# Kernel optimization log

Hardware: AMD Instinct MI355X
Metric: run time of the kernel (lower is better)

The kernel has to match this reference:

```python
import jax, jax.numpy as jnp
import numpy as np

N_CLASS, EMB, NH = 32000, 256, 512
B, T = 128, 256


def setup_inputs() -> dict:
    key = jax.random.key(0)
    ks = jax.random.split(key, 16)
    s_e = 1.0 / np.sqrt(EMB)
    s_h = 1.0 / np.sqrt(NH)
    inp = {
        "X": jax.random.randint(ks[0], (B, T), 0, N_CLASS),
        "H": jax.random.normal(ks[1], (B, NH), jnp.float32),
        "C": jax.random.normal(ks[2], (B, NH), jnp.float32),
        "E": jax.random.normal(ks[3], (N_CLASS, EMB), jnp.float32),
        # Linear weights stored as (in, out) so forward is x @ W
        "Wxf": jax.random.normal(ks[4], (EMB, NH), jnp.float32) * s_e,
        "Whf": jax.random.normal(ks[5], (NH, NH), jnp.float32) * s_h,
        "bf": jnp.ones((NH,), jnp.float32),
        "Wxi": jax.random.normal(ks[6], (EMB, NH), jnp.float32) * s_e,
        "Whi": jax.random.normal(ks[7], (NH, NH), jnp.float32) * s_h,
        "bi": jnp.ones((NH,), jnp.float32),
        "Wxc": jax.random.normal(ks[8], (EMB, NH), jnp.float32) * s_e,
        "Whc": jax.random.normal(ks[9], (NH, NH), jnp.float32) * s_h,
        "bc": jnp.ones((NH,), jnp.float32),
        "Wxo": jax.random.normal(ks[10], (EMB, NH), jnp.float32) * s_e,
        "Who": jax.random.normal(ks[11], (NH, NH), jnp.float32) * s_h,
        "bo": jnp.ones((NH,), jnp.float32),
        "Whq": jax.random.normal(ks[12], (NH, N_CLASS), jnp.float32) * s_h,
        "bq": jnp.ones((N_CLASS,), jnp.float32),
    }
    return inp


def reference(X, H, C, E, Wxf, Whf, bf, Wxi, Whi, bi, Wxc, Whc, bc,
              Wxo, Who, bo, Whq, bq):
    Xe = E[X]                      # [B, T, EMB]
    Xe = jnp.swapaxes(Xe, 0, 1)    # [T, B, EMB]
    # Precompute all input-side gate projections in one big GEMM pass.
    Wx = jnp.concatenate([Wxf, Wxi, Wxc, Wxo], axis=1)   # [EMB, 4*NH]
    gx = jnp.einsum('tbe,eg->tbg', Xe, Wx)               # [T, B, 4*NH]

    def step(carry, gxt):
        H, C = carry
        gf, gi, gc, go = jnp.split(gxt, 4, axis=-1)
        Ft = jax.nn.sigmoid(gf + H @ Whf + bf)
        It = jax.nn.sigmoid(gi + H @ Whi + bi)
        Ct = jnp.tanh(gc + H @ Whc + bc)
        Ot = jax.nn.sigmoid(go + H @ Who + bo)
        # NOTE: original code updates H with the OLD C, then updates C.
        Hn = Ot * jnp.tanh(C)
        Cn = Ft * C + It * Ct
        return (Hn, Cn), None

    (H, C), _ = jax.lax.scan(step, (H, C), gx)
    return H @ Whq + bq            # [B, N_CLASS]
```

## Files before the change

kernel.cpp:

```cpp
#include <hip/hip_runtime.h>
#include <stdint.h>

#define NCLASS 32000
#define EMB    256
#define NH     512
#define BATCH  128
#define TSEQ   256
#define G4     2048
#define NGROUP 8
#define NSLICE 32
#define GROWS  16

typedef _Float16 f16;
typedef _Float16 half8  __attribute__((ext_vector_type(8)));
typedef _Float16 half4v __attribute__((ext_vector_type(4)));
typedef float    float4v __attribute__((ext_vector_type(4)));

__device__ __forceinline__ float sigm(float x) { return 1.f / (1.f + __expf(-x)); }
__device__ __forceinline__ float ftanh(float x) {
    float a = fabsf(x);
    float e = __expf(2.f * a);
    float r = 1.f - 2.f / (e + 1.f);
    return copysignf(r, x);
}

#define GLOAD64_SC0(dst, ap) asm volatile("global_load_dwordx2 %0, %1, off sc0" : "=v"(dst) : "v"(ap))
#define GLOAD32_SC0(dst, ap) asm volatile("global_load_dword %0, %1, off sc0" : "=v"(dst) : "v"(ap))
#define GSTORE32_SC0(ap, val) asm volatile("global_store_dword %0, %1, off sc0" :: "v"(ap), "v"(val) : "memory")
#define WAITVM0() asm volatile("s_waitcnt vmcnt(0)" ::: "memory")


__global__ __launch_bounds__(256) void pack_wT(
    const float* __restrict__ Wf, const float* __restrict__ Wi,
    const float* __restrict__ Wc, const float* __restrict__ Wo,
    f16* __restrict__ WT, int K)
{
    int idx = blockIdx.x * 256 + threadIdx.x;
    if (idx >= G4 * K) return;
    int c = idx / K, k = idx - c * K;
    int j = c >> 2, g = c & 3;
    const float* W = (g == 0) ? Wf : ((g == 1) ? Wi : ((g == 2) ? Wc : Wo));
    WT[idx] = (f16)W[k * NH + j];
}

__global__ __launch_bounds__(256) void pack_bias(
    const float* __restrict__ bf_, const float* __restrict__ bi_,
    const float* __restrict__ bc_, const float* __restrict__ bo_,
    float* __restrict__ br)
{
    int c = blockIdx.x * 256 + threadIdx.x;
    if (c >= G4) return;
    int j = c >> 2, g = c & 3;
    const float* b = (g == 0) ? bf_ : ((g == 1) ? bi_ : ((g == 2) ? bc_ : bo_));
    br[c] = b[j];
}

__global__ __launch_bounds__(256) void transp_whq(
    const float* __restrict__ Whq, f16* __restrict__ WqT)
{
    __shared__ f16 T[64][72];
    int tid = threadIdx.x;
    int nb = blockIdx.x % (NCLASS / 64);
    int kb = blockIdx.x / (NCLASS / 64);
    int n0 = nb * 64, k0 = kb * 64;
    #pragma unroll
    for (int r = 0; r < 16; r++) {
        int id = tid + r * 256;
        int kr = id >> 6, nc = id & 63;
        T[nc][kr] = (f16)Whq[(size_t)(k0 + kr) * NCLASS + n0 + nc];
    }
    __syncthreads();
    #pragma unroll
    for (int r = 0; r < 2; r++) {
        int id = tid + r * 256;
        int nr = id >> 3, kc = (id & 7) * 8;
        *(half8*)&WqT[(size_t)(n0 + nr) * NH + k0 + kc] = *(half8*)&T[nr][kc];
    }
}

__global__ __launch_bounds__(256) void init_h(
    const float* __restrict__ H, f16* __restrict__ Hh)
{
    int i = blockIdx.x * 256 + threadIdx.x;
    if (i >= BATCH * NH) return;
    Hh[i] = (f16)H[i];
}

__global__ void zero_sync(int* s) { s[threadIdx.x] = 0; s[threadIdx.x + 256] = 0; }

__global__ __launch_bounds__(256) void lstm_persist(
    const int* __restrict__ X, const float* __restrict__ E,
    const float* __restrict__ C0,
    const f16* __restrict__ WxT, const f16* __restrict__ WhT,
    const float* __restrict__ bias,
    f16* __restrict__ Hb0, f16* __restrict__ Hb1,
    int* __restrict__ sync)
{
    __shared__ f16 WhS[64][520];
    __shared__ f16 WxS[64][264];
    __shared__ f16 XeS[2][16][264];
    __shared__ f16 HS[16][520];
    __shared__ int sGrp[2];

    const int tid  = threadIdx.x;
    const int wave = tid >> 6, lane = tid & 63;
    const int lrow = lane & 15, lhi = lane >> 4;
    const int gg = lane & 3;
    const int uu = (lane >> 2) & 3;

    if (tid == 0) {
        uint32_t xcc;
        asm volatile("s_getreg_b32 %0, hwreg(HW_REG_XCC_ID)" : "=s"(xcc));
        int grp = (int)(xcc & 7);
        sGrp[0] = grp;
        sGrp[1] = atomicAdd(&sync[256 + grp * 32], 1);
    }
    __syncthreads();
    const int g  = sGrp[0];
    const int s  = sGrp[1] & 31;
    const int b0 = g * GROWS;
    const int c0 = s * 64;
    const int j0 = s * 16;
    int* fl = sync + g * NSLICE;

    #pragma unroll
    for (int r = 0; r < 16; r++) {
        int id = tid + r * 256;
        int row = id >> 6, ko = (id & 63) * 8;
        *(half8*)&WhS[row][ko] = *(const half8*)(WhT + (size_t)(c0 + row) * NH + ko);
    }
    #pragma unroll
    for (int r = 0; r < 8; r++) {
        int id = tid + r * 256;
        int row = id >> 5, ko = (id & 31) * 8;
        *(half8*)&WxS[row][ko] = *(const half8*)(WxT + (size_t)(c0 + row) * EMB + ko);
    }
    float cReg = C0[(size_t)(b0 + 4 * lhi + gg) * NH + j0 + wave * 4 + uu];
    const float bv = bias[c0 + wave * 16 + lrow];

    auto prefetch_xe = [&](int t, int slot) {
        #pragma unroll
        for (int r = 0; r < 4; r++) {
            int id = tid + r * 256;
            int row = id >> 6, k4 = id & 63;
            int xv = X[(size_t)(b0 + row) * TSEQ + t];
            float4v e = *(const float4v*)(E + (size_t)xv * EMB + k4 * 4);
            half4v h; h[0] = (f16)e[0]; h[1] = (f16)e[1]; h[2] = (f16)e[2]; h[3] = (f16)e[3];
            *(half4v*)&XeS[slot][row][k4 * 4] = h;
        }
    };

    float4v acc0, acc1, acc2, acc3;
    auto mfma_wx = [&](int slot) {
        acc0 = (float4v)0.f; acc1 = (float4v)0.f;
        acc2 = (float4v)0.f; acc3 = (float4v)0.f;
        const f16(*xp)[264] = XeS[slot];
        #pragma unroll
        for (int kk = 0; kk < EMB; kk += 128) {
            half8 a0 = *(const half8*)&xp[lrow][kk      + lhi * 8];
            half8 w0 = *(const half8*)&WxS[wave * 16 + lrow][kk      + lhi * 8];
            half8 a1 = *(const half8*)&xp[lrow][kk + 32 + lhi * 8];
            half8 w1 = *(const half8*)&WxS[wave * 16 + lrow][kk + 32 + lhi * 8];
            half8 a2 = *(const half8*)&xp[lrow][kk + 64 + lhi * 8];
            half8 w2 = *(const half8*)&WxS[wave * 16 + lrow][kk + 64 + lhi * 8];
            half8 a3 = *(const half8*)&xp[lrow][kk + 96 + lhi * 8];
            half8 w3 = *(const half8*)&WxS[wave * 16 + lrow][kk + 96 + lhi * 8];
            acc0 = __builtin_amdgcn_mfma_f32_16x16x32_f16(a0, w0, acc0, 0, 0, 0);
            acc1 = __builtin_amdgcn_mfma_f32_16x16x32_f16(a1, w1, acc1, 0, 0, 0);
            acc2 = __builtin_amdgcn_mfma_f32_16x16x32_f16(a2, w2, acc2, 0, 0, 0);
            acc3 = __builtin_amdgcn_mfma_f32_16x16x32_f16(a3, w3, acc3, 0, 0, 0);
        }
    };

    prefetch_xe(0, 0);
    __syncthreads();
    mfma_wx(0);
    prefetch_xe(1, 1);

    for (int t = 0; t < TSEQ; t++) {
        if (wave == 0) {
            uint64_t fap = (uint64_t)(fl + (lane & 31));
            int f;
            do {
                GLOAD32_SC0(f, fap);
                WAITVM0();
                if (lane >= 32) f = 0x7fffffff;
            } while (__all(f >= t) == 0);
        }
        __syncthreads();

        {
            const f16* hsrcp = (t & 1) ? Hb1 : Hb0;
            uint64_t hv0, hv1, hv2, hv3, hv4, hv5, hv6, hv7;
#define LDH(rr, vv) { const int id_ = tid + rr * 256; const int row_ = id_ >> 7, qc_ = id_ & 127; \
            uint64_t ap_ = (uint64_t)(hsrcp + (size_t)(b0 + row_) * NH + qc_ * 4); GLOAD64_SC0(vv, ap_); }
            LDH(0, hv0) LDH(1, hv1) LDH(2, hv2) LDH(3, hv3)
            LDH(4, hv4) LDH(5, hv5) LDH(6, hv6) LDH(7, hv7)
#undef LDH
            WAITVM0();
            __builtin_amdgcn_sched_barrier(0);
#define STH(rr, vv) { const int id_ = tid + rr * 256; const int row_ = id_ >> 7, qc_ = id_ & 127; \
            *(uint64_t*)((char*)&HS[row_][0] + (size_t)qc_ * 8) = vv; }
            STH(0, hv0) STH(1, hv1) STH(2, hv2) STH(3, hv3)
            STH(4, hv4) STH(5, hv5) STH(6, hv6) STH(7, hv7)
#undef STH
        }
        __syncthreads();

        #pragma unroll
        for (int kk = 0; kk < NH; kk += 128) {
            half8 a0 = *(const half8*)&HS[lrow][kk      + lhi * 8];
            half8 w0 = *(const half8*)&WhS[wave * 16 + lrow][kk      + lhi * 8];
            half8 a1 = *(const half8*)&HS[lrow][kk + 32 + lhi * 8];
            half8 w1 = *(const half8*)&WhS[wave * 16 + lrow][kk + 32 + lhi * 8];
            half8 a2 = *(const half8*)&HS[lrow][kk + 64 + lhi * 8];
            half8 w2 = *(const half8*)&WhS[wave * 16 + lrow][kk + 64 + lhi * 8];
            half8 a3 = *(const half8*)&HS[lrow][kk + 96 + lhi * 8];
            half8 w3 = *(const half8*)&WhS[wave * 16 + lrow][kk + 96 + lhi * 8];
            acc0 = __builtin_amdgcn_mfma_f32_16x16x32_f16(a0, w0, acc0, 0, 0, 0);
            acc1 = __builtin_amdgcn_mfma_f32_16x16x32_f16(a1, w1, acc1, 0, 0, 0);
            acc2 = __builtin_amdgcn_mfma_f32_16x16x32_f16(a2, w2, acc2, 0, 0, 0);
            acc3 = __builtin_amdgcn_mfma_f32_16x16x32_f16(a3, w3, acc3, 0, 0, 0);
        }

        {
            float4v ssum = acc0 + acc1 + acc2 + acc3;
            ssum[0] += bv; ssum[1] += bv; ssum[2] += bv; ssum[3] += bv;
            float sg  = gg == 0 ? ssum[0] : gg == 1 ? ssum[1] : gg == 2 ? ssum[2] : ssum[3];
            float sg1 = gg == 0 ? ssum[1] : gg == 1 ? ssum[0] : gg == 2 ? ssum[3] : ssum[2];
            float sg2 = gg == 0 ? ssum[2] : gg == 1 ? ssum[3] : gg == 2 ? ssum[0] : ssum[1];
            float sg3 = gg == 0 ? ssum[3] : gg == 1 ? ssum[2] : gg == 2 ? ssum[1] : ssum[0];
            float r1 = __shfl_xor(sg1, 1);
            float r2 = __shfl_xor(sg2, 2);
            float r3 = __shfl_xor(sg3, 3);
            float F  = gg == 0 ? sg : gg == 1 ? r1 : gg == 2 ? r2 : r3;
            float I  = gg == 0 ? r1 : gg == 1 ? sg : gg == 2 ? r3 : r2;
            float Cc = gg == 0 ? r2 : gg == 1 ? r3 : gg == 2 ? sg : r1;
            float O  = gg == 0 ? r3 : gg == 1 ? r2 : gg == 2 ? r1 : sg;

            float Hn = sigm(O) * ftanh(cReg);
            cReg = sigm(F) * cReg + sigm(I) * ftanh(Cc);

            float Hp = __shfl_xor(Hn, 4);
            if ((lane & 4) == 0) {
                union { f16 h[2]; uint32_t u32; } pk;
                pk.h[0] = (f16)Hn; pk.h[1] = (f16)Hp;
                f16* hb = ((t + 1) & 1) ? Hb1 : Hb0;
                const int brow = b0 + 4 * lhi + gg;
                const int jcol = j0 + wave * 4 + uu;
                uint64_t ap = (uint64_t)(hb + (size_t)brow * NH + jcol);
                GSTORE32_SC0(ap, pk.u32);
            }
        }
        WAITVM0();
        __syncthreads();

        if (tid == 0)
            GSTORE32_SC0((uint64_t)&fl[s], t + 1);

        if (t + 1 < TSEQ) {
            mfma_wx((t + 1) & 1);
            if (t + 2 < TSEQ) prefetch_xe(t + 2, t & 1);
        }
    }
}

__global__ __launch_bounds__(256) void gemm_out(
    const f16* __restrict__ Hh, const f16* __restrict__ WqT,
    const float* __restrict__ bq, float* __restrict__ out)
{
    __shared__ f16 As[128][40];
    __shared__ f16 BsT[64][40];
    int tid = threadIdx.x, wave = tid >> 6, lane = tid & 63;
    int lrow = lane & 15, lhi = lane >> 4;
    int col0 = blockIdx.x * 64;

    float4v acc[2][4];
    #pragma unroll
    for (int m = 0; m < 2; m++)
        #pragma unroll
        for (int j = 0; j < 4; j++) acc[m][j] = (float4v)0.f;

    int ar = tid >> 1, ako = (tid & 1) * 16;
    int br = tid >> 2, bko = (tid & 3) * 8;
    for (int kk = 0; kk < NH; kk += 32) {
        *(half8*)&As[ar][ako]     = *(const half8*)(Hh + (size_t)ar * NH + kk + ako);
        *(half8*)&As[ar][ako + 8] = *(const half8*)(Hh + (size_t)ar * NH + kk + ako + 8);
        *(half8*)&BsT[br][bko]    = *(const half8*)(WqT + (size_t)(col0 + br) * NH + kk + bko);
        __syncthreads();
        half8 af[2];
        #pragma unroll
        for (int m = 0; m < 2; m++)
            af[m] = *(const half8*)&As[wave * 32 + m * 16 + lrow][lhi * 8];
        #pragma unroll
        for (int j = 0; j < 4; j++) {
            half8 bfr = *(const half8*)&BsT[j * 16 + lrow][lhi * 8];
            #pragma unroll
            for (int m = 0; m < 2; m++)
                acc[m][j] = __builtin_amdgcn_mfma_f32_16x16x32_f16(af[m], bfr, acc[m][j], 0, 0, 0);
        }
        __syncthreads();
    }
    #pragma unroll
    for (int m = 0; m < 2; m++)
        #pragma unroll
        for (int j = 0; j < 4; j++) {
            int col = col0 + j * 16 + lrow;
            float bqv = bq[col];
            #pragma unroll
            for (int r = 0; r < 4; r++) {
                int row = wave * 32 + m * 16 + lhi * 4 + r;
                out[(size_t)row * NCLASS + col] = acc[m][j][r] + bqv;
            }
        }
}

extern "C" void kernel_launch(void* const* d_in, const int* in_sizes, int n_in,
                              void* d_out, int out_size, void* d_ws, size_t ws_size,
                              hipStream_t stream)
{
    (void)in_sizes; (void)n_in; (void)out_size;
    const int*   X   = (const int*)  d_in[0];
    const float* H0  = (const float*)d_in[1];
    const float* C0  = (const float*)d_in[2];
    const float* E   = (const float*)d_in[3];
    const float* Wxf = (const float*)d_in[4];
    const float* Whf = (const float*)d_in[5];
    const float* bf_ = (const float*)d_in[6];
    const float* Wxi = (const float*)d_in[7];
    const float* Whi = (const float*)d_in[8];
    const float* bi_ = (const float*)d_in[9];
    const float* Wxc = (const float*)d_in[10];
    const float* Whc = (const float*)d_in[11];
    const float* bc_ = (const float*)d_in[12];
    const float* Wxo = (const float*)d_in[13];
    const float* Who = (const float*)d_in[14];
    const float* bo_ = (const float*)d_in[15];
    const float* Whq = (const float*)d_in[16];
    const float* bq  = (const float*)d_in[17];

    char* ws = (char*)d_ws;
    size_t o = 0;
    auto alloc = [&](size_t bytes) {
        size_t r = o;
        o = (o + bytes + 255) & ~(size_t)255;
        return r;
    };
    f16*   WxT  = (f16*)  (ws + alloc((size_t)G4 * EMB * 2));
    f16*   WhT  = (f16*)  (ws + alloc((size_t)G4 * NH * 2));
    float* bias = (float*)(ws + alloc((size_t)G4 * 4));
    f16*   WqT  = (f16*)  (ws + alloc((size_t)NH * NCLASS * 2));
    f16*   Hb0  = (f16*)  (ws + alloc((size_t)BATCH * NH * 2));
    f16*   Hb1  = (f16*)  (ws + alloc((size_t)BATCH * NH * 2));
    int*   sync = (int*)  (ws + alloc(512 * 4));
    if (o > ws_size) return;

    pack_wT  <<<(G4 * EMB + 255) / 256, 256, 0, stream>>>(Wxf, Wxi, Wxc, Wxo, WxT, EMB);
    pack_wT  <<<(G4 * NH  + 255) / 256, 256, 0, stream>>>(Whf, Whi, Whc, Who, WhT, NH);
    pack_bias<<<(G4 + 255) / 256,       256, 0, stream>>>(bf_, bi_, bc_, bo_, bias);
    transp_whq<<<(NCLASS / 64) * (NH / 64), 256, 0, stream>>>(Whq, WqT);
    init_h   <<<(BATCH * NH + 255) / 256, 256, 0, stream>>>(H0, Hb0);
    zero_sync<<<1, 256, 0, stream>>>(sync);

    lstm_persist<<<256, 256, 0, stream>>>(X, E, C0, WxT, WhT, bias, Hb0, Hb1, sync);

    gemm_out<<<NCLASS / 64, 256, 0, stream>>>(Hb0, WqT, bq, (float*)d_out);
}
```

Before: 668.1 us.

## Fuse prep kernels into one launch and convert Whq inside output GEMM

Merges the weight-packing, bias-packing, H init and sync-zero kernels into a single launch partitioned by block index. It also drops the separate Whq transpose/convert pass and its workspace buffer: the output GEMM now reads fp32 Whq directly, converts to fp16 and transposes into shared memory on the fly. This removes several launches and one full read-write round trip of the 64MB Whq matrix. In exchange, the GEMM reads twice the bytes for B and does scattered scalar LDS stores, which may cause bank conflicts.

```diff
diff --git a/kernel.cpp b/kernel.cpp
--- a/kernel.cpp
+++ b/kernel.cpp
@@ -29,64 +29,43 @@
 #define GSTORE32_SC0(ap, val) asm volatile("global_store_dword %0, %1, off sc0" :: "v"(ap), "v"(val) : "memory")
 #define WAITVM0() asm volatile("s_waitcnt vmcnt(0)" ::: "memory")
 
-
-__global__ __launch_bounds__(256) void pack_wT(
-    const float* __restrict__ Wf, const float* __restrict__ Wi,
-    const float* __restrict__ Wc, const float* __restrict__ Wo,
-    f16* __restrict__ WT, int K)
-{
-    int idx = blockIdx.x * 256 + threadIdx.x;
-    if (idx >= G4 * K) return;
-    int c = idx / K, k = idx - c * K;
-    int j = c >> 2, g = c & 3;
-    const float* W = (g == 0) ? Wf : ((g == 1) ? Wi : ((g == 2) ? Wc : Wo));
-    WT[idx] = (f16)W[k * NH + j];
-}
-
-__global__ __launch_bounds__(256) void pack_bias(
+__global__ __launch_bounds__(256) void mega_pack(
+    const float* __restrict__ Wxf, const float* __restrict__ Wxi,
+    const float* __restrict__ Wxc, const float* __restrict__ Wxo,
+    const float* __restrict__ Whf, const float* __restrict__ Whi,
+    const float* __restrict__ Whc, const float* __restrict__ Who,
     const float* __restrict__ bf_, const float* __restrict__ bi_,
     const float* __restrict__ bc_, const float* __restrict__ bo_,
-    float* __restrict__ br)
+    const float* __restrict__ H0,
+    f16* __restrict__ WxT, f16* __restrict__ WhT,
+    float* __restrict__ bias, f16* __restrict__ Hh, int* __restrict__ sync)
 {
-    int c = blockIdx.x * 256 + threadIdx.x;
-    if (c >= G4) return;
-    int j = c >> 2, g = c & 3;
-    const float* b = (g == 0) ? bf_ : ((g == 1) ? bi_ : ((g == 2) ? bc_ : bo_));
-    br[c] = b[j];
-}
-
-__global__ __launch_bounds__(256) void transp_whq(
-    const float* __restrict__ Whq, f16* __restrict__ WqT)
-{
-    __shared__ f16 T[64][72];
-    int tid = threadIdx.x;
-    int nb = blockIdx.x % (NCLASS / 64);
-    int kb = blockIdx.x / (NCLASS / 64);
-    int n0 = nb * 64, k0 = kb * 64;
-    #pragma unroll
-    for (int r = 0; r < 16; r++) {
-        int id = tid + r * 256;
-        int kr = id >> 6, nc = id & 63;
-        T[nc][kr] = (f16)Whq[(size_t)(k0 + kr) * NCLASS + n0 + nc];
-    }
-    __syncthreads();
-    #pragma unroll
-    for (int r = 0; r < 2; r++) {
-        int id = tid + r * 256;
-        int nr = id >> 3, kc = (id & 7) * 8;
-        *(half8*)&WqT[(size_t)(n0 + nr) * NH + k0 + kc] = *(half8*)&T[nr][kc];
-    }
-}
-
-__global__ __launch_bounds__(256) void init_h(
-    const float* __restrict__ H, f16* __restrict__ Hh)
-{
-    int i = blockIdx.x * 256 + threadIdx.x;
-    if (i >= BATCH * NH) return;
-    Hh[i] = (f16)H[i];
-}
-
-__global__ void zero_sync(int* s) { s[threadIdx.x] = 0; s[threadIdx.x + 256] = 0; }
+    const int bid = blockIdx.x, tid = threadIdx.x;
+    if (bid < 4096) {
+        int idx = bid * 256 + tid;
+        int c = idx >> 9, k = idx & 511;
+        int j = c >> 2, g = c & 3;
+        const float* W = (g == 0) ? Whf : ((g == 1) ? Whi : ((g == 2) ? Whc : Who));
+        WhT[idx] = (f16)W[k * NH + j];
+    } else if (bid < 6144) {
+        int idx = (bid - 4096) * 256 + tid;
+        int c = idx >> 8, k = idx & 255;
+        int j = c >> 2, g = c & 3;
+        const float* W = (g == 0) ? Wxf : ((g == 1) ? Wxi : ((g == 2) ? Wxc : Wxo));
+        WxT[idx] = (f16)W[k * NH + j];
+    } else if (bid < 6152) {
+        int c = (bid - 6144) * 256 + tid;
+        int j = c >> 2, g = c & 3;
+        const float* b = (g == 0) ? bf_ : ((g == 1) ? bi_ : ((g == 2) ? bc_ : bo_));
+        bias[c] = b[j];
+    } else if (bid < 6408) {
+        int i = (bid - 6152) * 256 + tid;
+        Hh[i] = (f16)H0[i];
+    } else {
+        sync[tid] = 0;
+        sync[tid + 256] = 0;
+    }
+}
 
 __global__ __launch_bounds__(256) void lstm_persist(
     const int* __restrict__ X, const float* __restrict__ E,
@@ -266,7 +245,7 @@
 }
 
 __global__ __launch_bounds__(256) void gemm_out(
-    const f16* __restrict__ Hh, const f16* __restrict__ WqT,
+    const f16* __restrict__ Hh, const float* __restrict__ Whq,
     const float* __restrict__ bq, float* __restrict__ out)
 {
     __shared__ f16 As[128][40];
@@ -282,11 +261,19 @@
         for (int j = 0; j < 4; j++) acc[m][j] = (float4v)0.f;
 
     int ar = tid >> 1, ako = (tid & 1) * 16;
-    int br = tid >> 2, bko = (tid & 3) * 8;
+    int kq = tid >> 3, n0q = (tid & 7) * 8;
     for (int kk = 0; kk < NH; kk += 32) {
         *(half8*)&As[ar][ako]     = *(const half8*)(Hh + (size_t)ar * NH + kk + ako);
         *(half8*)&As[ar][ako + 8] = *(const half8*)(Hh + (size_t)ar * NH + kk + ako + 8);
-        *(half8*)&BsT[br][bko]    = *(const half8*)(WqT + (size_t)(col0 + br) * NH + kk + bko);
+        {
+            const float* wsrc = Whq + (size_t)(kk + kq) * NCLASS + col0 + n0q;
+            float4v w0 = *(const float4v*)(wsrc);
+            float4v w1 = *(const float4v*)(wsrc + 4);
+            BsT[n0q + 0][kq] = (f16)w0[0]; BsT[n0q + 1][kq] = (f16)w0[1];
+            BsT[n0q + 2][kq] = (f16)w0[2]; BsT[n0q + 3][kq] = (f16)w0[3];
+            BsT[n0q + 4][kq] = (f16)w1[0]; BsT[n0q + 5][kq] = (f16)w1[1];
+            BsT[n0q + 6][kq] = (f16)w1[2]; BsT[n0q + 7][kq] = (f16)w1[3];
+        }
         __syncthreads();
         half8 af[2];
         #pragma unroll
@@ -349,20 +336,16 @@
     f16*   WxT  = (f16*)  (ws + alloc((size_t)G4 * EMB * 2));
     f16*   WhT  = (f16*)  (ws + alloc((size_t)G4 * NH * 2));
     float* bias = (float*)(ws + alloc((size_t)G4 * 4));
-    f16*   WqT  = (f16*)  (ws + alloc((size_t)NH * NCLASS * 2));
     f16*   Hb0  = (f16*)  (ws + alloc((size_t)BATCH * NH * 2));
     f16*   Hb1  = (f16*)  (ws + alloc((size_t)BATCH * NH * 2));
     int*   sync = (int*)  (ws + alloc(512 * 4));
     if (o > ws_size) return;
 
-    pack_wT  <<<(G4 * EMB + 255) / 256, 256, 0, stream>>>(Wxf, Wxi, Wxc, Wxo, WxT, EMB);
-    pack_wT  <<<(G4 * NH  + 255) / 256, 256, 0, stream>>>(Whf, Whi, Whc, Who, WhT, NH);
-    pack_bias<<<(G4 + 255) / 256,       256, 0, stream>>>(bf_, bi_, bc_, bo_, bias);
-    transp_whq<<<(NCLASS / 64) * (NH / 64), 256, 0, stream>>>(Whq, WqT);
-    init_h   <<<(BATCH * NH + 255) / 256, 256, 0, stream>>>(H0, Hb0);
-    zero_sync<<<1, 256, 0, stream>>>(sync);
+    mega_pack<<<6409, 256, 0, stream>>>(Wxf, Wxi, Wxc, Wxo, Whf, Whi, Whc, Who,
+                                        bf_, bi_, bc_, bo_, H0,
+                                        WxT, WhT, bias, Hb0, sync);
 
     lstm_persist<<<256, 256, 0, stream>>>(X, E, C0, WxT, WhT, bias, Hb0, Hb1, sync);
 
-    gemm_out<<<NCLASS / 64, 256, 0, stream>>>(Hb0, WqT, bq, (float*)d_out);
-}
+    gemm_out<<<NCLASS / 64, 256, 0, stream>>>(Hb0, Whq, bq, (float*)d_out);
+}
```

Measured after the change: 651.7 us. 1.03x faster.
